# Kernel tuning notes

Hardware: AMD Instinct MI355X
Metric: run time of the kernel (lower is better)

The kernel has to match this reference:

```python
import jax, jax.numpy as jnp
import numpy as np
from jax import lax

N, CIN, COUT, H, W = 16, 512, 256, 32, 32
EPS = 1e-5


def _conv(x, w, b, pad_h, pad_w):
    # x: [N,Cin,H,W], w: [Cout,Cin,kh,kw], pad = ((top,bottom),(left,right))
    y = lax.conv_general_dilated(
        x, w, window_strides=(1, 1), padding=(pad_h, pad_w),
        dimension_numbers=("NCHW", "OIHW", "NCHW"))
    return y + b[None, :, None, None]


def setup_inputs() -> dict:
    key = jax.random.key(0)
    ks = jax.random.split(key, 12)
    s = 0.02
    return {
        "x": jax.random.normal(ks[0], (N, CIN, H, W), jnp.float32),
        "w1": jax.random.normal(ks[1], (COUT, CIN, 3, 3), jnp.float32) * s,
        "b1": jax.random.normal(ks[2], (COUT,), jnp.float32) * s,
        "w2": jax.random.normal(ks[3], (COUT, CIN, 2, 3), jnp.float32) * s,
        "b2": jax.random.normal(ks[4], (COUT,), jnp.float32) * s,
        "w3": jax.random.normal(ks[5], (COUT, CIN, 3, 2), jnp.float32) * s,
        "b3": jax.random.normal(ks[6], (COUT,), jnp.float32) * s,
        "w4": jax.random.normal(ks[7], (COUT, CIN, 2, 2), jnp.float32) * s,
        "b4": jax.random.normal(ks[8], (COUT,), jnp.float32) * s,
        "gamma": jnp.ones((COUT,), jnp.float32),
        "beta": jnp.zeros((COUT,), jnp.float32),
    }


def reference(x, w1, b1, w2, b2, w3, b3, w4, b4, gamma, beta):
    # torch F.pad(l,r,t,b) -> lax padding ((top,bottom),(left,right))
    o1 = _conv(x, w1, b1, (1, 1), (1, 1))  # 3x3, pad (1,1,1,1) -> [N,Cout,H,W]
    o2 = _conv(x, w2, b2, (1, 0), (1, 1))  # 2x3, pad (1,1,1,0)
    o3 = _conv(x, w3, b3, (1, 1), (1, 0))  # 3x2, pad (1,0,1,1)
    o4 = _conv(x, w4, b4, (1, 0), (1, 0))  # 2x2, pad (1,0,1,0)
    # pixel-shuffle interleave: o1->(even,even), o2->(odd,even), o3->(even,odd), o4->(odd,odd)
    row_even = jnp.stack([o1, o3], axis=-1).reshape(N, COUT, H, 2 * W)
    row_odd = jnp.stack([o2, o4], axis=-1).reshape(N, COUT, H, 2 * W)
    y = jnp.stack([row_even, row_odd], axis=-2).reshape(N, COUT, 2 * H, 2 * W)
    # BatchNorm2d, training mode: biased batch stats over (N,H,W)
    mean = jnp.mean(y, axis=(0, 2, 3), keepdims=True)
    var = jnp.mean(jnp.square(y - mean), axis=(0, 2, 3), keepdims=True)
    normed = (y - mean) * lax.rsqrt(var + EPS)
    normed = normed * gamma[None, :, None, None] + beta[None, :, None, None]
    return jax.nn.relu(normed)
```

## Files before the change

kernel.cpp:

```cpp
#include <hip/hip_runtime.h>
#include <hip/hip_bf16.h>


typedef unsigned short ushort_t;
typedef __attribute__((ext_vector_type(8))) short short8;
typedef __attribute__((ext_vector_type(4))) float floatx4;
typedef __attribute__((ext_vector_type(2))) float floatx2;
typedef __attribute__((ext_vector_type(4))) unsigned short u16x4;
typedef __attribute__((ext_vector_type(8))) unsigned short u16x8;
typedef __attribute__((ext_vector_type(4))) unsigned int u32x4;

#define XT_OFF    0u
#define WT_OFF    18939904u
#define BIAS_OFF  28377088u
#define STATS_OFF 28381184u

#define NSITES_P0 204
#define NSITES_P1 170

#define ASYNC16(g, l) __builtin_amdgcn_global_load_lds( \
    (const __attribute__((address_space(1))) void*)(g), \
    (__attribute__((address_space(3))) void*)(l), 16, 0, 0)

__device__ __forceinline__ ushort_t f2bf(float f) {
  unsigned int u = __builtin_bit_cast(unsigned int, f);
  u += 0x7fffu + ((u >> 16) & 1u);
  return (ushort_t)(u >> 16);
}

__global__ __launch_bounds__(256) void prep_all(
    const float* __restrict__ x, ushort_t* __restrict__ xt,
    const float* __restrict__ w1, const float* __restrict__ w2,
    const float* __restrict__ w3, const float* __restrict__ w4,
    const float* __restrict__ b1, const float* __restrict__ b2,
    const float* __restrict__ b3, const float* __restrict__ b4,
    ushort_t* __restrict__ wt, float* __restrict__ bias,
    float* __restrict__ stats) {
  __shared__ ushort_t lds[128 * 36];
  const int blk = blockIdx.x;
  const int t = threadIdx.x;
  if (blk < 1024) {
    const int q = blk >> 8, co = blk & 255;
    const int row = ((q & 1) << 9) + (co << 1) + (q >> 1);
    if (blk == 0) { stats[t] = 0.f; stats[t + 256] = 0.f; }
    const float* wsrc; const float* bsrc; int khl, kwl;
    if (q == 0)      { wsrc = w1; bsrc = b1; khl = 3; kwl = 3; }
    else if (q == 1) { wsrc = w2; bsrc = b2; khl = 2; kwl = 3; }
    else if (q == 2) { wsrc = w3; bsrc = b3; khl = 3; kwl = 2; }
    else             { wsrc = w4; bsrc = b4; khl = 2; kwl = 2; }
    if (t == 0) bias[row] = bsrc[co];
    ushort_t* dst = wt + (size_t)row * 4608;
    for (int tap = 0; tap < 9; ++tap) {
      const int dh = tap / 3, dw = tap % 3;
      const bool valid = (dh < khl) && (dw < kwl);
#pragma unroll
      for (int cc = 0; cc < 2; ++cc) {
        const int ci = cc * 256 + t;
        ushort_t v = 0;
        if (valid)
          v = f2bf(wsrc[(((size_t)co * 512 + ci) * khl + dh) * kwl + dw]);
        dst[tap * 512 + ci] = v;
      }
    }
    return;
  }
  const int b = blk - 1024;
  const int n = b / 34, hp = b % 34;
  ushort_t* dst = xt + (size_t)(n * 34 + hp) * (34 * 512);
  if (hp == 0 || hp == 33) {
    u32x4 z = {0u, 0u, 0u, 0u};
    for (int i = t; i < 2176; i += 256) ((u32x4*)dst)[i] = z;
    return;
  }
  const int h = hp - 1;
  {
    u32x4 z = {0u, 0u, 0u, 0u};
    if (t < 64) ((u32x4*)dst)[t] = z;
    else if (t < 128) ((u32x4*)(dst + 33 * 512))[t - 64] = z;
  }
  const size_t base = (size_t)n * 524288 + (size_t)h * 32;
  for (int ci0 = 0; ci0 < 512; ci0 += 128) {
    __syncthreads();
    {
      const int cil = t >> 3;
      const int w4 = (t & 7) << 2;
#pragma unroll
      for (int cc = 0; cc < 4; ++cc) {
        const int ci = cil + cc * 32;
        floatx4 v = *(const floatx4*)(x + base + (size_t)(ci0 + ci) * 1024 + w4);
        u16x4 hv;
#pragma unroll
        for (int j = 0; j < 4; ++j) hv[j] = f2bf(v[j]);
        *(u16x4*)&lds[ci * 36 + w4] = hv;
      }
    }
    __syncthreads();
    {
      const int w = t & 31;
      const int j8 = t >> 5;
#pragma unroll
      for (int cc2 = 0; cc2 < 2; ++cc2) {
        const int cil = cc2 * 64 + j8 * 8;
        u16x8 v;
#pragma unroll
        for (int j = 0; j < 8; ++j) v[j] = lds[(cil + j) * 36 + w];
        *(u16x8*)(dst + (w + 1) * 512 + ci0 + cil) = v;
      }
    }
  }
}

template <int NTAPS, int NSITES_T>
__device__ __forceinline__ void gemm_body(
    const ushort_t* __restrict__ xt, const ushort_t* __restrict__ wt,
    const float* __restrict__ bias, float* __restrict__ out,
    float* __restrict__ stats, char* ldsX, char* ldsW0, char* ldsW1,
    int bn, int bm) {
  const int tid = threadIdx.x;
  const int n0 = bn << 7;
  const int n_img = bm >> 3;
  const int h0p = (bm & 7) << 2;
  const int wv = tid >> 6, lane = tid & 63;
  const int ri = lane & 15, kg = lane >> 4;
  const int wm = (wv & 1) << 6, wn = (wv >> 1) << 6;

  constexpr int XTOT = NSITES_T * 8;
  constexpr int XFP = XTOT / 256;
  constexpr int XTL = XTOT - XFP * 256;

  const char* xgp[XFP + 1];
  char* xlp[XFP + 1];
  {
    const char* xg = (const char*)(xt + (size_t)(n_img * 34 + h0p) * (34 * 512));
#pragma unroll
    for (int p = 0; p < XFP + 1; ++p) {
      const int idx = p * 256 + tid;
      const int site = idx >> 3, slot = idx & 7;
      const int c = slot ^ (site & 7);
      xgp[p] = xg + site * 1024 + (c << 4);
      xlp[p] = ldsX + idx * 16;
    }
  }
  const char* wgp[4];
  char* wlp0[4];
  char* wlp1[4];
#pragma unroll
  for (int p = 0; p < 4; ++p) {
    const int idx = p * 256 + tid;
    const int row = idx >> 3, slot = idx & 7;
    const int c = slot ^ (row & 7);
    wgp[p] = (const char*)wt + (size_t)(n0 + row) * 9216 + (c << 4);
    wlp0[p] = ldsW0 + idx * 16;
    wlp1[p] = ldsW1 + idx * 16;
  }

  floatx4 acc[4][4] = {};

  int arow[4], bsite[4];
#pragma unroll
  for (int f = 0; f < 4; ++f) arow[f] = wn + (f << 4) + ri;
#pragma unroll
  for (int fj = 0; fj < 4; ++fj)
    bsite[fj] = ((wm >> 5) + (fj >> 1)) * 34 + ((fj & 1) << 4) + ri;

  for (int chunk = 0; chunk < 8; ++chunk) {
    const int cb = chunk << 7;
#pragma unroll
    for (int p = 0; p < XFP; ++p) ASYNC16(xgp[p] + cb, xlp[p]);
    if (tid < XTL) ASYNC16(xgp[XFP] + cb, xlp[XFP]);
#pragma unroll
    for (int p = 0; p < 4; ++p) ASYNC16(wgp[p] + cb, wlp0[p]);
    __syncthreads();
#pragma unroll
    for (int tap = 0; tap < NTAPS; ++tap) {
      if (tap + 1 < NTAPS) {
        const int noff = ((tap + 1) << 10) + cb;
        if (tap & 1) {
#pragma unroll
          for (int p = 0; p < 4; ++p) ASYNC16(wgp[p] + noff, wlp0[p]);
        } else {
#pragma unroll
          for (int p = 0; p < 4; ++p) ASYNC16(wgp[p] + noff, wlp1[p]);
        }
      }
      const char* wb = (tap & 1) ? ldsW1 : ldsW0;
      const int tsite = (tap / 3) * 34 + (tap % 3);
#pragma unroll
      for (int ks = 0; ks < 2; ++ks) {
        const int c = (ks << 2) + kg;
        short8 a4[4], b4[4];
#pragma unroll
        for (int f = 0; f < 4; ++f)
          a4[f] = *(const short8*)(wb + arow[f] * 128 +
                                   ((c ^ (arow[f] & 7)) << 4));
#pragma unroll
        for (int fj = 0; fj < 4; ++fj) {
          const int srow = bsite[fj] + tsite;
          b4[fj] = *(const short8*)(ldsX + srow * 128 + ((c ^ (srow & 7)) << 4));
        }
#pragma unroll
        for (int fi = 0; fi < 4; ++fi)
#pragma unroll
          for (int fj = 0; fj < 4; ++fj)
            acc[fi][fj] = __builtin_amdgcn_mfma_f32_16x16x32_bf16(
                a4[fi], b4[fj], acc[fi][fj], 0, 0, 0);
      }
      __syncthreads();
    }
  }

  const int quad = kg, colL = ri;
  const int dh6 = (bn >> 2) << 6;
#pragma unroll
  for (int fi = 0; fi < 4; ++fi) {
    const int rbase = n0 + wn + (fi << 4) + (quad << 2);
    const floatx4 bv = *(const floatx4*)(bias + rbase);
    const int co = (rbase & 511) >> 1;
    float sA = 0.f, s2A = 0.f, sB = 0.f, s2B = 0.f;
    float* ob = out + (((size_t)(n_img * 256 + co)) << 12) + dh6;
#pragma unroll
    for (int fj = 0; fj < 4; ++fj) {
      const int mb = wm + (fj << 4) + colL;
      const int h = h0p + (mb >> 5), w = mb & 31;
      const float v0 = acc[fi][fj][0] + bv[0];
      const float v1 = acc[fi][fj][1] + bv[1];
      const float v2 = acc[fi][fj][2] + bv[2];
      const float v3 = acc[fi][fj][3] + bv[3];
      sA += v0 + v1;
      s2A += v0 * v0 + v1 * v1;
      sB += v2 + v3;
      s2B += v2 * v2 + v3 * v3;
      float* p = ob + (h << 7) + (w << 1);
      floatx2 eA = {v0, v1};
      floatx2 eB = {v2, v3};
      *(floatx2*)p = eA;
      *(floatx2*)(p + 4096) = eB;
    }
#pragma unroll
    for (int off = 1; off < 16; off <<= 1) {
      sA += __shfl_xor(sA, off);
      s2A += __shfl_xor(s2A, off);
      sB += __shfl_xor(sB, off);
      s2B += __shfl_xor(s2B, off);
    }
    if (colL == 0) {
      atomicAdd(&stats[co], sA);
      atomicAdd(&stats[256 + co], s2A);
      atomicAdd(&stats[co + 1], sB);
      atomicAdd(&stats[256 + co + 1], s2B);
    }
  }
}

__global__ __launch_bounds__(256) void gemm_kernel(
    const ushort_t* __restrict__ xt, const ushort_t* __restrict__ wt,
    const float* __restrict__ bias, float* __restrict__ out,
    float* __restrict__ stats) {
  __shared__ char ldsX[NSITES_P0 * 128];
  __shared__ char ldsW[2][128 * 128];
  const int bx = blockIdx.x;
  const int bn = (bx & 7) ^ (((bx >> 9) & 1) << 2);
  const int bm = (bx >> 3) & 127;
  if (bn < 4)
    gemm_body<9, NSITES_P0>(xt, wt, bias, out, stats,
                            ldsX, ldsW[0], ldsW[1], bn, bm);
  else
    gemm_body<6, NSITES_P1>(xt, wt, bias, out, stats,
                            ldsX, ldsW[0], ldsW[1], bn, bm);
}

__global__ __launch_bounds__(256) void bn_apply(
    float* __restrict__ y, const float* __restrict__ stats,
    const float* __restrict__ gamma, const float* __restrict__ beta) {
  const int b = blockIdx.x;
  const int co = b & 255;
  const int t = threadIdx.x;
  const float mean = stats[co] * (1.f / 65536.f);
  const float var = stats[256 + co] * (1.f / 65536.f) - mean * mean;
  const float rstd = rsqrtf(var + 1e-5f);
  const float scale = rstd * gamma[co];
  const float shift = beta[co] - mean * scale;
  float* p = y + (size_t)b * 4096;
#pragma unroll
  for (int it = 0; it < 4; ++it) {
    floatx4* q = (floatx4*)(p + (it * 256 + t) * 4);
    floatx4 v = *q;
#pragma unroll
    for (int e = 0; e < 4; ++e) v[e] = fmaxf(v[e] * scale + shift, 0.f);
    *q = v;
  }
}

extern "C" void kernel_launch(void* const* d_in, const int* in_sizes, int n_in,
                              void* d_out, int out_size, void* d_ws,
                              size_t ws_size, hipStream_t stream) {
  const float* x  = (const float*)d_in[0];
  const float* w1 = (const float*)d_in[1];
  const float* b1 = (const float*)d_in[2];
  const float* w2 = (const float*)d_in[3];
  const float* b2 = (const float*)d_in[4];
  const float* w3 = (const float*)d_in[5];
  const float* b3 = (const float*)d_in[6];
  const float* w4 = (const float*)d_in[7];
  const float* b4 = (const float*)d_in[8];
  const float* gamma = (const float*)d_in[9];
  const float* beta  = (const float*)d_in[10];
  float* out = (float*)d_out;

  char* ws = (char*)d_ws;
  ushort_t* xt   = (ushort_t*)(ws + XT_OFF);
  ushort_t* wt   = (ushort_t*)(ws + WT_OFF);
  float*    bias = (float*)(ws + BIAS_OFF);
  float*    st   = (float*)(ws + STATS_OFF);

  prep_all<<<1568, 256, 0, stream>>>(x, xt, w1, w2, w3, w4,
                                     b1, b2, b3, b4, wt, bias, st);
  gemm_kernel<<<1024, 256, 0, stream>>>(xt, wt, bias, out, st);
  bn_apply<<<4096, 256, 0, stream>>>(out, st, gamma, beta);
}
```

Baseline: 271.1 us.

## Triple-buffer weight taps with partial vmcnt waits instead of full barriers

Moves the per-tap weight tile pipeline from double to triple buffering in LDS, prefetching two taps ahead. The __syncthreads calls become inline s_waitcnt vmcnt(4) plus s_barrier, so only the older tap's loads must land before compute continues. The aim is to hide global-to-LDS latency of the weight tiles behind MFMA work. In exchange it uses an extra 16 KB of LDS, which may lower occupancy, and the correctness of hand-counted vmcnt values depends on the order in which loads are issued.

```diff
diff --git a/kernel.cpp b/kernel.cpp
--- a/kernel.cpp
+++ b/kernel.cpp
@@ -21,6 +21,13 @@
 #define ASYNC16(g, l) __builtin_amdgcn_global_load_lds( \
     (const __attribute__((address_space(1))) void*)(g), \
     (__attribute__((address_space(3))) void*)(l), 16, 0, 0)
+
+#define ISSUE_FENCE asm volatile("" ::: "memory")
+
+#define WAITBAR4 \
+  asm volatile("s_waitcnt vmcnt(4) lgkmcnt(0)\n\ts_barrier" ::: "memory")
+#define WAITBAR0 \
+  asm volatile("s_waitcnt vmcnt(0) lgkmcnt(0)\n\ts_barrier" ::: "memory")
 
 __device__ __forceinline__ ushort_t f2bf(float f) {
   unsigned int u = __builtin_bit_cast(unsigned int, f);
@@ -114,7 +121,7 @@
 __device__ __forceinline__ void gemm_body(
     const ushort_t* __restrict__ xt, const ushort_t* __restrict__ wt,
     const float* __restrict__ bias, float* __restrict__ out,
-    float* __restrict__ stats, char* ldsX, char* ldsW0, char* ldsW1,
+    float* __restrict__ stats, char* ldsX, char* ldsW,
     int bn, int bm) {
   const int tid = threadIdx.x;
   const int n0 = bn << 7;
@@ -142,17 +149,14 @@
     }
   }
   const char* wgp[4];
-  char* wlp0[4];
-  char* wlp1[4];
 #pragma unroll
   for (int p = 0; p < 4; ++p) {
     const int idx = p * 256 + tid;
     const int row = idx >> 3, slot = idx & 7;
     const int c = slot ^ (row & 7);
     wgp[p] = (const char*)wt + (size_t)(n0 + row) * 9216 + (c << 4);
-    wlp0[p] = ldsW0 + idx * 16;
-    wlp1[p] = ldsW1 + idx * 16;
-  }
+  }
+  char* const wl = ldsW + tid * 16;
 
   floatx4 acc[4][4] = {};
 
@@ -168,22 +172,23 @@
 #pragma unroll
     for (int p = 0; p < XFP; ++p) ASYNC16(xgp[p] + cb, xlp[p]);
     if (tid < XTL) ASYNC16(xgp[XFP] + cb, xlp[XFP]);
-#pragma unroll
-    for (int p = 0; p < 4; ++p) ASYNC16(wgp[p] + cb, wlp0[p]);
-    __syncthreads();
+    ISSUE_FENCE;
+#pragma unroll
+    for (int p = 0; p < 4; ++p) ASYNC16(wgp[p] + cb, wl + p * 4096);
+    ISSUE_FENCE;
+#pragma unroll
+    for (int p = 0; p < 4; ++p)
+      ASYNC16(wgp[p] + cb + 1024, wl + 16384 + p * 4096);
+    WAITBAR4;
 #pragma unroll
     for (int tap = 0; tap < NTAPS; ++tap) {
-      if (tap + 1 < NTAPS) {
-        const int noff = ((tap + 1) << 10) + cb;
-        if (tap & 1) {
-#pragma unroll
-          for (int p = 0; p < 4; ++p) ASYNC16(wgp[p] + noff, wlp0[p]);
-        } else {
-#pragma unroll
-          for (int p = 0; p < 4; ++p) ASYNC16(wgp[p] + noff, wlp1[p]);
-        }
-      }
-      const char* wb = (tap & 1) ? ldsW1 : ldsW0;
+      if (tap + 2 < NTAPS) {
+        const int noff = ((tap + 2) << 10) + cb;
+        char* const wld = ldsW + ((tap + 2) % 3) * 16384 + tid * 16;
+#pragma unroll
+        for (int p = 0; p < 4; ++p) ASYNC16(wgp[p] + noff, wld + p * 4096);
+      }
+      const char* wb = ldsW + (tap % 3) * 16384;
       const int tsite = (tap / 3) * 34 + (tap % 3);
 #pragma unroll
       for (int ks = 0; ks < 2; ++ks) {
@@ -205,7 +210,7 @@
             acc[fi][fj] = __builtin_amdgcn_mfma_f32_16x16x32_bf16(
                 a4[fi], b4[fj], acc[fi][fj], 0, 0, 0);
       }
-      __syncthreads();
+      if (tap + 2 < NTAPS) { WAITBAR4; } else { WAITBAR0; }
     }
   }
 
@@ -257,16 +262,16 @@
     const float* __restrict__ bias, float* __restrict__ out,
     float* __restrict__ stats) {
   __shared__ char ldsX[NSITES_P0 * 128];
-  __shared__ char ldsW[2][128 * 128];
+  __shared__ char ldsW[3][128 * 128];
   const int bx = blockIdx.x;
   const int bn = (bx & 7) ^ (((bx >> 9) & 1) << 2);
   const int bm = (bx >> 3) & 127;
   if (bn < 4)
     gemm_body<9, NSITES_P0>(xt, wt, bias, out, stats,
-                            ldsX, ldsW[0], ldsW[1], bn, bm);
+                            ldsX, ldsW[0], bn, bm);
   else
     gemm_body<6, NSITES_P1>(xt, wt, bias, out, stats,
-                            ldsX, ldsW[0], ldsW[1], bn, bm);
+                            ldsX, ldsW[0], bn, bm);
 }
 
 __global__ __launch_bounds__(256) void bn_apply(
```

Result: faster. 264.4 us (-2.5%).
